# Optimization experiments

Hardware: AMD Instinct MI355X
Metric: run time of the kernel (lower is better)

The kernel has to match this reference:

```python
import jax, jax.numpy as jnp
import numpy as np

N = 100000
IN_C = 128
OUT_C = 128
E = 1600000


def setup_inputs() -> dict:
    key = jax.random.key(0)
    k1, k2, k3, k4 = jax.random.split(key, 4)
    x = jax.random.normal(k1, (N, IN_C), dtype=jnp.float32)
    edge_index = jax.random.randint(k2, (2, E), 0, N, dtype=jnp.int64)
    # GCNConv params: linear weight (stored [in, out] for x @ W) and bias [out]
    W = jax.random.normal(k3, (IN_C, OUT_C), dtype=jnp.float32) / np.sqrt(IN_C)
    b = jax.random.normal(k4, (OUT_C,), dtype=jnp.float32) * 0.01
    return {"x": x, "edge_index": edge_index, "W": W, "b": b}


def reference(x, edge_index, W, b):
    n = x.shape[0]
    # add self loops (PyG GCNConv default add_self_loops=True)
    loop = jnp.arange(n, dtype=edge_index.dtype)
    src = jnp.concatenate([edge_index[0], loop])  # message sources
    dst = jnp.concatenate([edge_index[1], loop])  # aggregation targets
    # symmetric normalization: deg over targets (edge weight 1, incl. self loops)
    deg = jax.ops.segment_sum(jnp.ones_like(dst, dtype=x.dtype), dst, num_segments=n)
    dinv = jnp.where(deg > 0, jax.lax.rsqrt(deg), 0.0)
    norm = dinv[src] * dinv[dst]  # [E+N]
    # linear transform then gather-scale-scatter aggregation
    h = x @ W  # [N, out]
    msgs = h[src] * norm[:, None]  # [E+N, out] -- dominant memory traffic
    out = jax.ops.segment_sum(msgs, dst, num_segments=n)
    return out + b
```

## Files before the change

### kernel.cpp

```cpp
#include <hip/hip_runtime.h>


#define SCAN_T 256
#define SCAN_E 1024
#define WPB 4
#define CAP 2560
#define SC_T 8192

typedef __attribute__((ext_vector_type(8))) short short8;
typedef __attribute__((ext_vector_type(4))) float f32x4;

__device__ __forceinline__ unsigned short f2bf(float f) {
  unsigned int u = __float_as_uint(f);
  u += 0x7FFFu + ((u >> 16) & 1u);
  return (unsigned short)(u >> 16);
}
__device__ __forceinline__ float bf_lo(unsigned int u) { return __uint_as_float(u << 16); }
__device__ __forceinline__ float bf_hi(unsigned int u) { return __uint_as_float(u & 0xFFFF0000u); }


__global__ void k_zero(int* __restrict__ p, int m) {
  int i = blockIdx.x * blockDim.x + threadIdx.x;
  if (i < m) p[i] = 0;
}

__global__ void __launch_bounds__(512) k_scatter(
    const int* __restrict__ ei, int* __restrict__ bcursor,
    int* __restrict__ pairs, int E, int B) {
  __shared__ int hist[1024];
  int t = threadIdx.x;
  for (int b = t; b < B; b += 512) hist[b] = 0;
  __syncthreads();
  int e0 = blockIdx.x * SC_T;
  int eend = min(e0 + SC_T, E);
  for (int e = e0 + t * 4; e < eend; e += 2048) {
    if (e + 3 < eend) {
      int4 d = *(const int4*)(ei + E + e);
      atomicAdd(&hist[((unsigned)d.x) >> 7], 1);
      atomicAdd(&hist[((unsigned)d.y) >> 7], 1);
      atomicAdd(&hist[((unsigned)d.z) >> 7], 1);
      atomicAdd(&hist[((unsigned)d.w) >> 7], 1);
    } else {
      for (int q = e; q < eend; ++q) atomicAdd(&hist[((unsigned)ei[E + q]) >> 7], 1);
    }
  }
  __syncthreads();
  for (int b = t; b < B; b += 512) {
    int c = hist[b];
    hist[b] = c ? atomicAdd(&bcursor[b], c) : 0;
  }
  __syncthreads();
  for (int e = e0 + t * 4; e < eend; e += 2048) {
    if (e + 3 < eend) {
      int4 s = *(const int4*)(ei + e);
      int4 d = *(const int4*)(ei + E + e);
      int b0 = ((unsigned)d.x) >> 7; int p0 = atomicAdd(&hist[b0], 1);
      if (p0 < CAP) pairs[(size_t)b0 * CAP + p0] = ((d.x & 127) << 17) | s.x;
      int b1 = ((unsigned)d.y) >> 7; int p1 = atomicAdd(&hist[b1], 1);
      if (p1 < CAP) pairs[(size_t)b1 * CAP + p1] = ((d.y & 127) << 17) | s.y;
      int b2 = ((unsigned)d.z) >> 7; int p2 = atomicAdd(&hist[b2], 1);
      if (p2 < CAP) pairs[(size_t)b2 * CAP + p2] = ((d.z & 127) << 17) | s.z;
      int b3 = ((unsigned)d.w) >> 7; int p3 = atomicAdd(&hist[b3], 1);
      if (p3 < CAP) pairs[(size_t)b3 * CAP + p3] = ((d.w & 127) << 17) | s.w;
    } else {
      for (int q = e; q < eend; ++q) {
        int dst = ei[E + q], src = ei[q];
        int b0 = ((unsigned)dst) >> 7; int p0 = atomicAdd(&hist[b0], 1);
        if (p0 < CAP) pairs[(size_t)b0 * CAP + p0] = ((dst & 127) << 17) | src;
      }
    }
  }
}

__global__ void __launch_bounds__(256) k_gemm_hd(
    const float* __restrict__ x, const float* __restrict__ W,
    const int* __restrict__ pairs, const int* __restrict__ bcursor,
    unsigned short* __restrict__ h, int n) {
  __shared__ alignas(16) unsigned short Wt[128][136];
  __shared__ int hist[128];
  int t = threadIdx.x;
  int b = blockIdx.x;
  if (t < 128) hist[t] = 0;
  __syncthreads();
  int cnt = min(bcursor[b], CAP);
  const int* __restrict__ gp = pairs + (size_t)b * CAP;
  for (int i = t; i < cnt; i += 256) atomicAdd(&hist[gp[i] >> 17], 1);
#pragma unroll
  for (int p = 0; p < 16; ++p) {
    int task = p * 256 + t;
    int kg = task >> 7, nn = task & 127;
    float w0 = W[(kg * 4 + 0) * 128 + nn];
    float w1 = W[(kg * 4 + 1) * 128 + nn];
    float w2 = W[(kg * 4 + 2) * 128 + nn];
    float w3 = W[(kg * 4 + 3) * 128 + nn];
    ushort4 u;
    u.x = f2bf(w0); u.y = f2bf(w1); u.z = f2bf(w2); u.w = f2bf(w3);
    *(ushort4*)&Wt[nn][kg * 4] = u;
  }
  __syncthreads();
  int w = t >> 6, lane = t & 63;
  int q = lane >> 4, m = lane & 15;
#pragma unroll
  for (int rep = 0; rep < 2; ++rep) {
    int lbase = rep * 64 + w * 16;
    int r0 = (b << 7) + lbase;
    f32x4 acc[8];
#pragma unroll
    for (int nt = 0; nt < 8; ++nt) acc[nt] = (f32x4){0.f, 0.f, 0.f, 0.f};
    float dscale[4];
#pragma unroll
    for (int rg = 0; rg < 4; ++rg)
      dscale[rg] = rsqrtf((float)hist[lbase + q * 4 + rg] + 1.0f);
#pragma unroll
    for (int ks = 0; ks < 4; ++ks) {
      int row = r0 + m;
      row = row < n ? row : n - 1;
      const float* xp = x + (size_t)row * 128 + ks * 32 + q * 8;
      float4 a0 = *(const float4*)xp;
      float4 a1 = *(const float4*)(xp + 4);
      short8 af;
      af[0] = (short)f2bf(a0.x); af[1] = (short)f2bf(a0.y);
      af[2] = (short)f2bf(a0.z); af[3] = (short)f2bf(a0.w);
      af[4] = (short)f2bf(a1.x); af[5] = (short)f2bf(a1.y);
      af[6] = (short)f2bf(a1.z); af[7] = (short)f2bf(a1.w);
#pragma unroll
      for (int nt = 0; nt < 8; ++nt) {
        short8 bf = *(const short8*)&Wt[nt * 16 + m][ks * 32 + q * 8];
        acc[nt] = __builtin_amdgcn_mfma_f32_16x16x32_bf16(af, bf, acc[nt], 0, 0, 0);
      }
    }
#pragma unroll
    for (int nt = 0; nt < 8; ++nt)
#pragma unroll
      for (int rg = 0; rg < 4; ++rg) {
        int r = r0 + q * 4 + rg;
        if (r < n) h[(size_t)r * 128 + nt * 16 + m] = f2bf(acc[nt][rg] * dscale[rg]);
      }
  }
}

__global__ void __launch_bounds__(512) k_sort_agg(
    const int* __restrict__ pairs, const int* __restrict__ bcursor,
    const uint4* __restrict__ h4, const float* __restrict__ bias,
    float* __restrict__ out, int n) {
  __shared__ int sorted[CAP];
  __shared__ int hist[128], base_[128], cur[128];
  __shared__ int nextn;
  int t = threadIdx.x;
  int b = blockIdx.x;
  if (t < 128) { hist[t] = 0; cur[t] = 0; }
  if (t == 0) nextn = 0;
  __syncthreads();
  int cnt = min(bcursor[b], CAP);
  const int* __restrict__ gp = pairs + (size_t)b * CAP;
  for (int i = t; i < cnt; i += 512) atomicAdd(&hist[gp[i] >> 17], 1);
  __syncthreads();
  if (t < 128) base_[t] = hist[t];
  __syncthreads();
#pragma unroll
  for (int d = 1; d < 128; d <<= 1) {
    int v = (t < 128 && t >= d) ? base_[t - d] : 0;
    __syncthreads();
    if (t < 128) base_[t] += v;
    __syncthreads();
  }
  if (t < 128) base_[t] -= hist[t];
  __syncthreads();
  for (int i = t; i < cnt; i += 512) {
    int p = gp[i];
    int d = p >> 17;
    int pos = base_[d] + atomicAdd(&cur[d], 1);
    sorted[pos] = p & 0x1FFFF;
  }
  __syncthreads();

  int lane = t & 63;
  int ln = lane & 15;
  int nbase = b << 7;
  for (;;) {
    int row = 0;
    if (ln == 0) row = atomicAdd(&nextn, 1);
    row = __shfl(row, lane & 48, 64);
    if (row >= 128) break;
    int node = nbase + row;
    bool act = node < n;
    uint4 sp = make_uint4(0u, 0u, 0u, 0u);
    if (act) sp = h4[(size_t)node * 16 + ln];
    float a[8];
    a[0] = bf_lo(sp.x); a[1] = bf_hi(sp.x);
    a[2] = bf_lo(sp.y); a[3] = bf_hi(sp.y);
    a[4] = bf_lo(sp.z); a[5] = bf_hi(sp.z);
    a[6] = bf_lo(sp.w); a[7] = bf_hi(sp.w);
    int s = base_[row];
    int cd = hist[row];
    int end = s + cd;
    for (; s + 8 <= end; s += 8) {
      uint4 u[8];
#pragma unroll
      for (int k = 0; k < 8; ++k) {
        int idx = sorted[s + k];
        u[k] = h4[(size_t)idx * 16 + ln];
      }
#pragma unroll
      for (int k = 0; k < 8; ++k) {
        a[0] += bf_lo(u[k].x); a[1] += bf_hi(u[k].x);
        a[2] += bf_lo(u[k].y); a[3] += bf_hi(u[k].y);
        a[4] += bf_lo(u[k].z); a[5] += bf_hi(u[k].z);
        a[6] += bf_lo(u[k].w); a[7] += bf_hi(u[k].w);
      }
    }
    for (; s + 4 <= end; s += 4) {
      uint4 u[4];
#pragma unroll
      for (int k = 0; k < 4; ++k) {
        int idx = sorted[s + k];
        u[k] = h4[(size_t)idx * 16 + ln];
      }
#pragma unroll
      for (int k = 0; k < 4; ++k) {
        a[0] += bf_lo(u[k].x); a[1] += bf_hi(u[k].x);
        a[2] += bf_lo(u[k].y); a[3] += bf_hi(u[k].y);
        a[4] += bf_lo(u[k].z); a[5] += bf_hi(u[k].z);
        a[6] += bf_lo(u[k].w); a[7] += bf_hi(u[k].w);
      }
    }
    for (; s < end; ++s) {
      int idx = sorted[s];
      uint4 u = h4[(size_t)idx * 16 + ln];
      a[0] += bf_lo(u.x); a[1] += bf_hi(u.x);
      a[2] += bf_lo(u.y); a[3] += bf_hi(u.y);
      a[4] += bf_lo(u.z); a[5] += bf_hi(u.z);
      a[6] += bf_lo(u.w); a[7] += bf_hi(u.w);
    }
    if (act) {
      float di = rsqrtf((float)cd + 1.0f);
      float4 b0 = ((const float4*)bias)[2 * ln];
      float4 b1 = ((const float4*)bias)[2 * ln + 1];
      f32x4 r0, r1;
      r0[0] = fmaf(a[0], di, b0.x); r0[1] = fmaf(a[1], di, b0.y);
      r0[2] = fmaf(a[2], di, b0.z); r0[3] = fmaf(a[3], di, b0.w);
      r1[0] = fmaf(a[4], di, b1.x); r1[1] = fmaf(a[5], di, b1.y);
      r1[2] = fmaf(a[6], di, b1.z); r1[3] = fmaf(a[7], di, b1.w);
      f32x4* op = (f32x4*)(out + (size_t)node * 128 + ln * 8);
      __builtin_nontemporal_store(r0, op);
      __builtin_nontemporal_store(r1, op + 1);
    }
  }
}


__global__ void k_init(int* __restrict__ cnt, int n) {
  int i = blockIdx.x * blockDim.x + threadIdx.x;
  if (i < n) cnt[i] = 0;
}

__global__ void k_count4(const int* __restrict__ ei, int* __restrict__ cnt, int E) {
  int i = blockIdx.x * blockDim.x + threadIdx.x;
  int e = i * 4;
  if (e + 3 < E) {
    int4 d = *(const int4*)(ei + E + e);
    atomicAdd(&cnt[d.x], 1); atomicAdd(&cnt[d.y], 1);
    atomicAdd(&cnt[d.z], 1); atomicAdd(&cnt[d.w], 1);
  } else {
    for (; e < E; ++e) atomicAdd(&cnt[ei[E + e]], 1);
  }
}

__global__ void k_scan_local(const int* __restrict__ cnt, int* __restrict__ offs,
                             int* __restrict__ bsums, int n) {
  __shared__ int sh[SCAN_T];
  int t = threadIdx.x;
  int base = blockIdx.x * SCAN_E + t * 4;
  int v0 = 0, v1 = 0, v2 = 0, v3 = 0;
  if (base + 0 < n) v0 = cnt[base + 0];
  if (base + 1 < n) v1 = cnt[base + 1];
  if (base + 2 < n) v2 = cnt[base + 2];
  if (base + 3 < n) v3 = cnt[base + 3];
  int sum = v0 + v1 + v2 + v3;
  sh[t] = sum;
  __syncthreads();
  for (int d = 1; d < SCAN_T; d <<= 1) {
    int xv = (t >= d) ? sh[t - d] : 0;
    __syncthreads();
    sh[t] += xv;
    __syncthreads();
  }
  int run = sh[t] - sum;
  if (base + 0 < n) offs[base + 0] = run; run += v0;
  if (base + 1 < n) offs[base + 1] = run; run += v1;
  if (base + 2 < n) offs[base + 2] = run; run += v2;
  if (base + 3 < n) offs[base + 3] = run;
  if (t == SCAN_T - 1) bsums[blockIdx.x] = sh[t];
}

__global__ void k_scan_bsums(int* __restrict__ bsums, int nb) {
  __shared__ int sh[SCAN_T];
  int t = threadIdx.x;
  int v = (t < nb) ? bsums[t] : 0;
  sh[t] = v;
  __syncthreads();
  for (int d = 1; d < SCAN_T; d <<= 1) {
    int xv = (t >= d) ? sh[t - d] : 0;
    __syncthreads();
    sh[t] += xv;
    __syncthreads();
  }
  if (t < nb) bsums[t] = sh[t] - v;
}

__global__ void k_scan_finish(int* __restrict__ offs, const int* __restrict__ bsums,
                              const int* __restrict__ cnt, int* __restrict__ offs2,
                              float* __restrict__ dinv, int n) {
  int i = blockIdx.x * blockDim.x + threadIdx.x;
  if (i < n) {
    int o = offs[i] + bsums[i / SCAN_E];
    offs[i] = o;
    offs2[i] = o;
    dinv[i] = rsqrtf((float)cnt[i] + 1.0f);
  }
}

__global__ void k_fill4(const int* __restrict__ ei, int* __restrict__ offs2,
                        int* __restrict__ csr, int E) {
  int i = blockIdx.x * blockDim.x + threadIdx.x;
  int e = i * 4;
  if (e + 3 < E) {
    int4 s = *(const int4*)(ei + e);
    int4 d = *(const int4*)(ei + E + e);
    csr[atomicAdd(&offs2[d.x], 1)] = s.x;
    csr[atomicAdd(&offs2[d.y], 1)] = s.y;
    csr[atomicAdd(&offs2[d.z], 1)] = s.z;
    csr[atomicAdd(&offs2[d.w], 1)] = s.w;
  } else {
    for (; e < E; ++e) csr[atomicAdd(&offs2[ei[E + e]], 1)] = ei[e];
  }
}

__global__ void __launch_bounds__(256) k_gemm_h(
    const float* __restrict__ x, const float* __restrict__ W,
    const float* __restrict__ dinv, unsigned short* __restrict__ h, int n) {
  __shared__ alignas(16) unsigned short Wt[128][136];
  int t = threadIdx.x;
#pragma unroll
  for (int p = 0; p < 16; ++p) {
    int task = p * 256 + t;
    int kg = task >> 7, nn = task & 127;
    float w0 = W[(kg * 4 + 0) * 128 + nn];
    float w1 = W[(kg * 4 + 1) * 128 + nn];
    float w2 = W[(kg * 4 + 2) * 128 + nn];
    float w3 = W[(kg * 4 + 3) * 128 + nn];
    ushort4 u;
    u.x = f2bf(w0); u.y = f2bf(w1); u.z = f2bf(w2); u.w = f2bf(w3);
    *(ushort4*)&Wt[nn][kg * 4] = u;
  }
  __syncthreads();
  int w = t >> 6, lane = t & 63;
  int q = lane >> 4, m = lane & 15;
  int r0 = blockIdx.x * 64 + w * 16;
  f32x4 acc[8];
#pragma unroll
  for (int nt = 0; nt < 8; ++nt) acc[nt] = (f32x4){0.f, 0.f, 0.f, 0.f};
  float dscale[4];
#pragma unroll
  for (int rg = 0; rg < 4; ++rg) {
    int r = r0 + q * 4 + rg;
    dscale[rg] = dinv[r < n ? r : n - 1];
  }
#pragma unroll
  for (int ks = 0; ks < 4; ++ks) {
    int row = r0 + m;
    row = row < n ? row : n - 1;
    const float* xp = x + (size_t)row * 128 + ks * 32 + q * 8;
    float4 a0 = *(const float4*)xp;
    float4 a1 = *(const float4*)(xp + 4);
    short8 af;
    af[0] = (short)f2bf(a0.x); af[1] = (short)f2bf(a0.y);
    af[2] = (short)f2bf(a0.z); af[3] = (short)f2bf(a0.w);
    af[4] = (short)f2bf(a1.x); af[5] = (short)f2bf(a1.y);
    af[6] = (short)f2bf(a1.z); af[7] = (short)f2bf(a1.w);
#pragma unroll
    for (int nt = 0; nt < 8; ++nt) {
      short8 bf = *(const short8*)&Wt[nt * 16 + m][ks * 32 + q * 8];
      acc[nt] = __builtin_amdgcn_mfma_f32_16x16x32_bf16(af, bf, acc[nt], 0, 0, 0);
    }
  }
#pragma unroll
  for (int nt = 0; nt < 8; ++nt)
#pragma unroll
    for (int rg = 0; rg < 4; ++rg) {
      int r = r0 + q * 4 + rg;
      if (r < n) h[(size_t)r * 128 + nt * 16 + m] = f2bf(acc[nt][rg] * dscale[rg]);
    }
}

__global__ void __launch_bounds__(256) k_agg_bias_csr(
    const unsigned int* __restrict__ h2, const float* __restrict__ dinv,
    const int* __restrict__ offs, const int* __restrict__ cnt,
    const int* __restrict__ csr, const float* __restrict__ bias,
    float* __restrict__ out, int n) {
  int node = blockIdx.x * WPB + (threadIdx.x >> 6);
  int lane = threadIdx.x & 63;
  if (node >= n) return;
  unsigned int sp = h2[(size_t)node * 64 + lane];
  float ax = bf_lo(sp), ay = bf_hi(sp);
  int s = offs[node];
  int end = s + cnt[node];
  for (; s + 8 <= end; s += 8) {
    int i0 = csr[s + 0], i1 = csr[s + 1], i2 = csr[s + 2], i3 = csr[s + 3];
    int i4 = csr[s + 4], i5 = csr[s + 5], i6 = csr[s + 6], i7 = csr[s + 7];
    unsigned int u0 = h2[(size_t)i0 * 64 + lane];
    unsigned int u1 = h2[(size_t)i1 * 64 + lane];
    unsigned int u2 = h2[(size_t)i2 * 64 + lane];
    unsigned int u3 = h2[(size_t)i3 * 64 + lane];
    unsigned int u4 = h2[(size_t)i4 * 64 + lane];
    unsigned int u5 = h2[(size_t)i5 * 64 + lane];
    unsigned int u6 = h2[(size_t)i6 * 64 + lane];
    unsigned int u7 = h2[(size_t)i7 * 64 + lane];
    ax += (bf_lo(u0) + bf_lo(u1)) + (bf_lo(u2) + bf_lo(u3)) +
          (bf_lo(u4) + bf_lo(u5)) + (bf_lo(u6) + bf_lo(u7));
    ay += (bf_hi(u0) + bf_hi(u1)) + (bf_hi(u2) + bf_hi(u3)) +
          (bf_hi(u4) + bf_hi(u5)) + (bf_hi(u6) + bf_hi(u7));
  }
  for (; s < end; ++s) {
    unsigned int u = h2[(size_t)csr[s] * 64 + lane];
    ax += bf_lo(u); ay += bf_hi(u);
  }
  float di = dinv[node];
  float2 bb = ((const float2*)bias)[lane];
  float2 r;
  r.x = fmaf(ax, di, bb.x);
  r.y = fmaf(ay, di, bb.y);
  ((float2*)out)[(size_t)node * 64 + lane] = r;
}

extern "C" void kernel_launch(void* const* d_in, const int* in_sizes, int n_in,
                              void* d_out, int out_size, void* d_ws, size_t ws_size,
                              hipStream_t stream) {
  const float* x = (const float*)d_in[0];
  const int* ei = (const int*)d_in[1];
  const float* Wm = (const float*)d_in[2];
  const float* bias = (const float*)d_in[3];
  float* out = (float*)d_out;

  int N = in_sizes[0] / 128;
  int E = in_sizes[1] / 2;
  int NB64 = (N + 63) >> 6;
  int NB128 = (N + 127) >> 7;

  int nb_n = (N + 255) / 256;
  int nb_e4 = ((E + 3) / 4 + 255) / 256;

  size_t off_pairs = 4096;
  size_t off_h = (off_pairs + (size_t)NB128 * CAP * 4 + 255) & ~(size_t)255;
  size_t need14 = off_h + (size_t)N * 256;

  if (ws_size >= need14 && N <= (1 << 17) && NB128 <= 1024) {
    char* p = (char*)d_ws;
    int* bcursor = (int*)p;
    int* pairs = (int*)(p + off_pairs);
    unsigned short* h = (unsigned short*)(p + off_h);

    k_zero<<<4, 256, 0, stream>>>(bcursor, 1024);
    k_scatter<<<(E + SC_T - 1) / SC_T, 512, 0, stream>>>(ei, bcursor, pairs, E, NB128);
    k_gemm_hd<<<NB128, 256, 0, stream>>>(x, Wm, pairs, bcursor, h, N);
    k_sort_agg<<<NB128, 512, 0, stream>>>(pairs, bcursor, (const uint4*)h, bias, out, N);
    return;
  }

  char* p = (char*)d_ws;
  int* cnt = (int*)p;        p += (size_t)N * 4;
  int* offs = (int*)p;       p += (size_t)N * 4;
  int* offs2 = (int*)p;      p += (size_t)N * 4;
  float* dinv = (float*)p;   p += (size_t)N * 4;
  int* bsums = (int*)p;      p += 1024;
  int* csr = (int*)p;        p += (size_t)E * 4;
  unsigned short* h = (unsigned short*)p;

  int nb_scan = (N + SCAN_E - 1) / SCAN_E;

  k_init<<<nb_n, 256, 0, stream>>>(cnt, N);
  k_count4<<<nb_e4, 256, 0, stream>>>(ei, cnt, E);
  k_scan_local<<<nb_scan, SCAN_T, 0, stream>>>(cnt, offs, bsums, N);
  k_scan_bsums<<<1, SCAN_T, 0, stream>>>(bsums, nb_scan);
  k_scan_finish<<<nb_n, 256, 0, stream>>>(offs, bsums, cnt, offs2, dinv, N);
  k_fill4<<<nb_e4, 256, 0, stream>>>(ei, offs2, csr, E);
  k_gemm_h<<<NB64, 256, 0, stream>>>(x, Wm, dinv, h, N);
  k_agg_bias_csr<<<(N + WPB - 1) / WPB, 256, 0, stream>>>(
      (const unsigned int*)h, dinv, offs, cnt, csr, bias, out, N);
}
```

Baseline: 204.3 us.

## Run edge scatter and GEMM concurrently in one launch, apply source norm in aggregation

Merges the edge bucketing scatter and the x@W GEMM into a single kernel, with block ranges assigned to each role, so the two independent stages can overlap on the GPU. The GEMM no longer depends on degree counts, so the source-side normalization moves out of h. A new small k_deg kernel writes dinv per node, and the aggregation gathers dinv[src] per edge and multiplies it in with an FMA. This adds a per-edge scalar gather and an extra launch, and GEMM blocks now have 512 threads each handling 128 rows.

```diff
diff --git a/kernel.cpp b/kernel.cpp
--- a/kernel.cpp
+++ b/kernel.cpp
@@ -24,93 +24,79 @@
   if (i < m) p[i] = 0;
 }
 
-__global__ void __launch_bounds__(512) k_scatter(
+__global__ void __launch_bounds__(512) k_scat_gemm(
     const int* __restrict__ ei, int* __restrict__ bcursor,
-    int* __restrict__ pairs, int E, int B) {
-  __shared__ int hist[1024];
+    int* __restrict__ pairs, int E, int B, int NSC,
+    const float* __restrict__ x, const float* __restrict__ W,
+    unsigned short* __restrict__ h, int n) {
+  __shared__ alignas(16) unsigned char smem_raw[128 * 136 * 2];
   int t = threadIdx.x;
-  for (int b = t; b < B; b += 512) hist[b] = 0;
-  __syncthreads();
-  int e0 = blockIdx.x * SC_T;
-  int eend = min(e0 + SC_T, E);
-  for (int e = e0 + t * 4; e < eend; e += 2048) {
-    if (e + 3 < eend) {
-      int4 d = *(const int4*)(ei + E + e);
-      atomicAdd(&hist[((unsigned)d.x) >> 7], 1);
-      atomicAdd(&hist[((unsigned)d.y) >> 7], 1);
-      atomicAdd(&hist[((unsigned)d.z) >> 7], 1);
-      atomicAdd(&hist[((unsigned)d.w) >> 7], 1);
-    } else {
-      for (int q = e; q < eend; ++q) atomicAdd(&hist[((unsigned)ei[E + q]) >> 7], 1);
-    }
-  }
-  __syncthreads();
-  for (int b = t; b < B; b += 512) {
-    int c = hist[b];
-    hist[b] = c ? atomicAdd(&bcursor[b], c) : 0;
-  }
-  __syncthreads();
-  for (int e = e0 + t * 4; e < eend; e += 2048) {
-    if (e + 3 < eend) {
-      int4 s = *(const int4*)(ei + e);
-      int4 d = *(const int4*)(ei + E + e);
-      int b0 = ((unsigned)d.x) >> 7; int p0 = atomicAdd(&hist[b0], 1);
-      if (p0 < CAP) pairs[(size_t)b0 * CAP + p0] = ((d.x & 127) << 17) | s.x;
-      int b1 = ((unsigned)d.y) >> 7; int p1 = atomicAdd(&hist[b1], 1);
-      if (p1 < CAP) pairs[(size_t)b1 * CAP + p1] = ((d.y & 127) << 17) | s.y;
-      int b2 = ((unsigned)d.z) >> 7; int p2 = atomicAdd(&hist[b2], 1);
-      if (p2 < CAP) pairs[(size_t)b2 * CAP + p2] = ((d.z & 127) << 17) | s.z;
-      int b3 = ((unsigned)d.w) >> 7; int p3 = atomicAdd(&hist[b3], 1);
-      if (p3 < CAP) pairs[(size_t)b3 * CAP + p3] = ((d.w & 127) << 17) | s.w;
-    } else {
-      for (int q = e; q < eend; ++q) {
-        int dst = ei[E + q], src = ei[q];
-        int b0 = ((unsigned)dst) >> 7; int p0 = atomicAdd(&hist[b0], 1);
-        if (p0 < CAP) pairs[(size_t)b0 * CAP + p0] = ((dst & 127) << 17) | src;
-      }
-    }
-  }
-}
-
-__global__ void __launch_bounds__(256) k_gemm_hd(
-    const float* __restrict__ x, const float* __restrict__ W,
-    const int* __restrict__ pairs, const int* __restrict__ bcursor,
-    unsigned short* __restrict__ h, int n) {
-  __shared__ alignas(16) unsigned short Wt[128][136];
-  __shared__ int hist[128];
-  int t = threadIdx.x;
-  int b = blockIdx.x;
-  if (t < 128) hist[t] = 0;
-  __syncthreads();
-  int cnt = min(bcursor[b], CAP);
-  const int* __restrict__ gp = pairs + (size_t)b * CAP;
-  for (int i = t; i < cnt; i += 256) atomicAdd(&hist[gp[i] >> 17], 1);
-#pragma unroll
-  for (int p = 0; p < 16; ++p) {
-    int task = p * 256 + t;
-    int kg = task >> 7, nn = task & 127;
-    float w0 = W[(kg * 4 + 0) * 128 + nn];
-    float w1 = W[(kg * 4 + 1) * 128 + nn];
-    float w2 = W[(kg * 4 + 2) * 128 + nn];
-    float w3 = W[(kg * 4 + 3) * 128 + nn];
-    ushort4 u;
-    u.x = f2bf(w0); u.y = f2bf(w1); u.z = f2bf(w2); u.w = f2bf(w3);
-    *(ushort4*)&Wt[nn][kg * 4] = u;
-  }
-  __syncthreads();
-  int w = t >> 6, lane = t & 63;
-  int q = lane >> 4, m = lane & 15;
-#pragma unroll
-  for (int rep = 0; rep < 2; ++rep) {
-    int lbase = rep * 64 + w * 16;
-    int r0 = (b << 7) + lbase;
+  if ((int)blockIdx.x < NSC) {
+    int* hist = (int*)smem_raw;
+    for (int b = t; b < B; b += 512) hist[b] = 0;
+    __syncthreads();
+    int e0 = blockIdx.x * SC_T;
+    int eend = min(e0 + SC_T, E);
+    for (int e = e0 + t * 4; e < eend; e += 2048) {
+      if (e + 3 < eend) {
+        int4 d = *(const int4*)(ei + E + e);
+        atomicAdd(&hist[((unsigned)d.x) >> 7], 1);
+        atomicAdd(&hist[((unsigned)d.y) >> 7], 1);
+        atomicAdd(&hist[((unsigned)d.z) >> 7], 1);
+        atomicAdd(&hist[((unsigned)d.w) >> 7], 1);
+      } else {
+        for (int q = e; q < eend; ++q) atomicAdd(&hist[((unsigned)ei[E + q]) >> 7], 1);
+      }
+    }
+    __syncthreads();
+    for (int b = t; b < B; b += 512) {
+      int c = hist[b];
+      hist[b] = c ? atomicAdd(&bcursor[b], c) : 0;
+    }
+    __syncthreads();
+    for (int e = e0 + t * 4; e < eend; e += 2048) {
+      if (e + 3 < eend) {
+        int4 s = *(const int4*)(ei + e);
+        int4 d = *(const int4*)(ei + E + e);
+        int b0 = ((unsigned)d.x) >> 7; int p0 = atomicAdd(&hist[b0], 1);
+        if (p0 < CAP) pairs[(size_t)b0 * CAP + p0] = ((d.x & 127) << 17) | s.x;
+        int b1 = ((unsigned)d.y) >> 7; int p1 = atomicAdd(&hist[b1], 1);
+        if (p1 < CAP) pairs[(size_t)b1 * CAP + p1] = ((d.y & 127) << 17) | s.y;
+        int b2 = ((unsigned)d.z) >> 7; int p2 = atomicAdd(&hist[b2], 1);
+        if (p2 < CAP) pairs[(size_t)b2 * CAP + p2] = ((d.z & 127) << 17) | s.z;
+        int b3 = ((unsigned)d.w) >> 7; int p3 = atomicAdd(&hist[b3], 1);
+        if (p3 < CAP) pairs[(size_t)b3 * CAP + p3] = ((d.w & 127) << 17) | s.w;
+      } else {
+        for (int q = e; q < eend; ++q) {
+          int dst = ei[E + q], src = ei[q];
+          int b0 = ((unsigned)dst) >> 7; int p0 = atomicAdd(&hist[b0], 1);
+          if (p0 < CAP) pairs[(size_t)b0 * CAP + p0] = ((dst & 127) << 17) | src;
+        }
+      }
+    }
+  } else {
+    typedef unsigned short WtRow[136];
+    WtRow* Wt = (WtRow*)smem_raw;
+    int bb = blockIdx.x - NSC;
+#pragma unroll
+    for (int p = 0; p < 8; ++p) {
+      int task = p * 512 + t;
+      int kg = task >> 7, nn = task & 127;
+      float w0 = W[(kg * 4 + 0) * 128 + nn];
+      float w1 = W[(kg * 4 + 1) * 128 + nn];
+      float w2 = W[(kg * 4 + 2) * 128 + nn];
+      float w3 = W[(kg * 4 + 3) * 128 + nn];
+      ushort4 u;
+      u.x = f2bf(w0); u.y = f2bf(w1); u.z = f2bf(w2); u.w = f2bf(w3);
+      *(ushort4*)&Wt[nn][kg * 4] = u;
+    }
+    __syncthreads();
+    int w = t >> 6, lane = t & 63;
+    int q = lane >> 4, m = lane & 15;
+    int r0 = (bb << 7) + w * 16;
     f32x4 acc[8];
 #pragma unroll
     for (int nt = 0; nt < 8; ++nt) acc[nt] = (f32x4){0.f, 0.f, 0.f, 0.f};
-    float dscale[4];
-#pragma unroll
-    for (int rg = 0; rg < 4; ++rg)
-      dscale[rg] = rsqrtf((float)hist[lbase + q * 4 + rg] + 1.0f);
 #pragma unroll
     for (int ks = 0; ks < 4; ++ks) {
       int row = r0 + m;
@@ -134,15 +120,33 @@
 #pragma unroll
       for (int rg = 0; rg < 4; ++rg) {
         int r = r0 + q * 4 + rg;
-        if (r < n) h[(size_t)r * 128 + nt * 16 + m] = f2bf(acc[nt][rg] * dscale[rg]);
-      }
+        if (r < n) h[(size_t)r * 128 + nt * 16 + m] = f2bf(acc[nt][rg]);
+      }
+  }
+}
+
+__global__ void __launch_bounds__(256) k_deg(
+    const int* __restrict__ pairs, const int* __restrict__ bcursor,
+    float* __restrict__ dinv, int n) {
+  __shared__ int hist[128];
+  int t = threadIdx.x;
+  int b = blockIdx.x;
+  if (t < 128) hist[t] = 0;
+  __syncthreads();
+  int cnt = min(bcursor[b], CAP);
+  const int* __restrict__ gp = pairs + (size_t)b * CAP;
+  for (int i = t; i < cnt; i += 256) atomicAdd(&hist[gp[i] >> 17], 1);
+  __syncthreads();
+  if (t < 128) {
+    int node = b * 128 + t;
+    if (node < n) dinv[node] = rsqrtf((float)hist[t] + 1.0f);
   }
 }
 
 __global__ void __launch_bounds__(512) k_sort_agg(
     const int* __restrict__ pairs, const int* __restrict__ bcursor,
-    const uint4* __restrict__ h4, const float* __restrict__ bias,
-    float* __restrict__ out, int n) {
+    const uint4* __restrict__ h4, const float* __restrict__ dinv,
+    const float* __restrict__ bias, float* __restrict__ out, int n) {
   __shared__ int sorted[CAP];
   __shared__ int hist[128], base_[128], cur[128];
   __shared__ int nextn;
@@ -184,63 +188,66 @@
     if (row >= 128) break;
     int node = nbase + row;
     bool act = node < n;
+    int cd = hist[row];
+    float did = rsqrtf((float)cd + 1.0f);
     uint4 sp = make_uint4(0u, 0u, 0u, 0u);
     if (act) sp = h4[(size_t)node * 16 + ln];
     float a[8];
-    a[0] = bf_lo(sp.x); a[1] = bf_hi(sp.x);
-    a[2] = bf_lo(sp.y); a[3] = bf_hi(sp.y);
-    a[4] = bf_lo(sp.z); a[5] = bf_hi(sp.z);
-    a[6] = bf_lo(sp.w); a[7] = bf_hi(sp.w);
+    a[0] = did * bf_lo(sp.x); a[1] = did * bf_hi(sp.x);
+    a[2] = did * bf_lo(sp.y); a[3] = did * bf_hi(sp.y);
+    a[4] = did * bf_lo(sp.z); a[5] = did * bf_hi(sp.z);
+    a[6] = did * bf_lo(sp.w); a[7] = did * bf_hi(sp.w);
     int s = base_[row];
-    int cd = hist[row];
     int end = s + cd;
     for (; s + 8 <= end; s += 8) {
-      uint4 u[8];
+      uint4 u[8]; float dv[8];
 #pragma unroll
       for (int k = 0; k < 8; ++k) {
         int idx = sorted[s + k];
         u[k] = h4[(size_t)idx * 16 + ln];
+        dv[k] = dinv[idx];
       }
 #pragma unroll
       for (int k = 0; k < 8; ++k) {
-        a[0] += bf_lo(u[k].x); a[1] += bf_hi(u[k].x);
-        a[2] += bf_lo(u[k].y); a[3] += bf_hi(u[k].y);
-        a[4] += bf_lo(u[k].z); a[5] += bf_hi(u[k].z);
-        a[6] += bf_lo(u[k].w); a[7] += bf_hi(u[k].w);
+        a[0] = fmaf(bf_lo(u[k].x), dv[k], a[0]); a[1] = fmaf(bf_hi(u[k].x), dv[k], a[1]);
+        a[2] = fmaf(bf_lo(u[k].y), dv[k], a[2]); a[3] = fmaf(bf_hi(u[k].y), dv[k], a[3]);
+        a[4] = fmaf(bf_lo(u[k].z), dv[k], a[4]); a[5] = fmaf(bf_hi(u[k].z), dv[k], a[5]);
+        a[6] = fmaf(bf_lo(u[k].w), dv[k], a[6]); a[7] = fmaf(bf_hi(u[k].w), dv[k], a[7]);
       }
     }
     for (; s + 4 <= end; s += 4) {
-      uint4 u[4];
+      uint4 u[4]; float dv[4];
 #pragma unroll
       for (int k = 0; k < 4; ++k) {
         int idx = sorted[s + k];
         u[k] = h4[(size_t)idx * 16 + ln];
+        dv[k] = dinv[idx];
       }
 #pragma unroll
       for (int k = 0; k < 4; ++k) {
-        a[0] += bf_lo(u[k].x); a[1] += bf_hi(u[k].x);
-        a[2] += bf_lo(u[k].y); a[3] += bf_hi(u[k].y);
-        a[4] += bf_lo(u[k].z); a[5] += bf_hi(u[k].z);
-        a[6] += bf_lo(u[k].w); a[7] += bf_hi(u[k].w);
+        a[0] = fmaf(bf_lo(u[k].x), dv[k], a[0]); a[1] = fmaf(bf_hi(u[k].x), dv[k], a[1]);
+        a[2] = fmaf(bf_lo(u[k].y), dv[k], a[2]); a[3] = fmaf(bf_hi(u[k].y), dv[k], a[3]);
+        a[4] = fmaf(bf_lo(u[k].z), dv[k], a[4]); a[5] = fmaf(bf_hi(u[k].z), dv[k], a[5]);
+        a[6] = fmaf(bf_lo(u[k].w), dv[k], a[6]); a[7] = fmaf(bf_hi(u[k].w), dv[k], a[7]);
       }
     }
     for (; s < end; ++s) {
       int idx = sorted[s];
       uint4 u = h4[(size_t)idx * 16 + ln];
-      a[0] += bf_lo(u.x); a[1] += bf_hi(u.x);
-      a[2] += bf_lo(u.y); a[3] += bf_hi(u.y);
-      a[4] += bf_lo(u.z); a[5] += bf_hi(u.z);
-      a[6] += bf_lo(u.w); a[7] += bf_hi(u.w);
+      float dv = dinv[idx];
+      a[0] = fmaf(bf_lo(u.x), dv, a[0]); a[1] = fmaf(bf_hi(u.x), dv, a[1]);
+      a[2] = fmaf(bf_lo(u.y), dv, a[2]); a[3] = fmaf(bf_hi(u.y), dv, a[3]);
+      a[4] = fmaf(bf_lo(u.z), dv, a[4]); a[5] = fmaf(bf_hi(u.z), dv, a[5]);
+      a[6] = fmaf(bf_lo(u.w), dv, a[6]); a[7] = fmaf(bf_hi(u.w), dv, a[7]);
     }
     if (act) {
-      float di = rsqrtf((float)cd + 1.0f);
       float4 b0 = ((const float4*)bias)[2 * ln];
       float4 b1 = ((const float4*)bias)[2 * ln + 1];
       f32x4 r0, r1;
-      r0[0] = fmaf(a[0], di, b0.x); r0[1] = fmaf(a[1], di, b0.y);
-      r0[2] = fmaf(a[2], di, b0.z); r0[3] = fmaf(a[3], di, b0.w);
-      r1[0] = fmaf(a[4], di, b1.x); r1[1] = fmaf(a[5], di, b1.y);
-      r1[2] = fmaf(a[6], di, b1.z); r1[3] = fmaf(a[7], di, b1.w);
+      r0[0] = fmaf(a[0], did, b0.x); r0[1] = fmaf(a[1], did, b0.y);
+      r0[2] = fmaf(a[2], did, b0.z); r0[3] = fmaf(a[3], did, b0.w);
+      r1[0] = fmaf(a[4], did, b1.x); r1[1] = fmaf(a[5], did, b1.y);
+      r1[2] = fmaf(a[6], did, b1.z); r1[3] = fmaf(a[7], did, b1.w);
       f32x4* op = (f32x4*)(out + (size_t)node * 128 + ln * 8);
       __builtin_nontemporal_store(r0, op);
       __builtin_nontemporal_store(r1, op + 1);
@@ -452,18 +459,23 @@
 
   size_t off_pairs = 4096;
   size_t off_h = (off_pairs + (size_t)NB128 * CAP * 4 + 255) & ~(size_t)255;
-  size_t need14 = off_h + (size_t)N * 256;
-
-  if (ws_size >= need14 && N <= (1 << 17) && NB128 <= 1024) {
+  size_t off_dinv = (off_h + (size_t)N * 256 + 255) & ~(size_t)255;
+  size_t need17 = off_dinv + (size_t)N * 4;
+
+  if (ws_size >= need17 && N <= (1 << 17) && NB128 <= 1024) {
     char* p = (char*)d_ws;
     int* bcursor = (int*)p;
     int* pairs = (int*)(p + off_pairs);
     unsigned short* h = (unsigned short*)(p + off_h);
-
+    float* dinv = (float*)(p + off_dinv);
+
+    int NSC = (E + SC_T - 1) / SC_T;
     k_zero<<<4, 256, 0, stream>>>(bcursor, 1024);
-    k_scatter<<<(E + SC_T - 1) / SC_T, 512, 0, stream>>>(ei, bcursor, pairs, E, NB128);
-    k_gemm_hd<<<NB128, 256, 0, stream>>>(x, Wm, pairs, bcursor, h, N);
-    k_sort_agg<<<NB128, 512, 0, stream>>>(pairs, bcursor, (const uint4*)h, bias, out, N);
+    k_scat_gemm<<<NSC + NB128, 512, 0, stream>>>(
+        ei, bcursor, pairs, E, NB128, NSC, x, Wm, h, N);
+    k_deg<<<NB128, 256, 0, stream>>>(pairs, bcursor, dinv, N);
+    k_sort_agg<<<NB128, 512, 0, stream>>>(
+        pairs, bcursor, (const uint4*)h, dinv, bias, out, N);
     return;
   }
 
```

Result: faster. 199.5 us (-2.3%).
